# Optimization experiments

Hardware: AMD Instinct MI355X
Metric: run time of the kernel (lower is better)

The kernel has to match this reference:

```python
import jax, jax.numpy as jnp
import numpy as np
import itertools, math

MODES = 10
PHOTONS = 5
_IN_MODES_NP = np.arange(0, MODES, 2)  # input_state = [1,0,1,0,...]: photons in even modes
IN_MODES = jnp.asarray(_IN_MODES_NP)

# ---- Ryser's formula constants for 5x5 permanents (2^5 = 32 column subsets) ----
P = PHOTONS
_SUBS = np.array([[(s >> j) & 1 for j in range(P)] for s in range(1 << P)], dtype=np.float32)
_SIGNS = np.array([(-1.0) ** (P - bin(s).count('1')) for s in range(1 << P)], dtype=np.float32)
SUBS_C = jnp.asarray(_SUBS).astype(jnp.complex64)   # (32, P)
SIGNS = jnp.asarray(_SIGNS)                          # (32,)


def permanents(A):
    """Batched permanent via Ryser. A: (..., P, P) complex64 -> (...,) complex64."""
    # row sums over each column subset: (..., 32, P)
    rs = jnp.einsum('...rc,sc->...sr', A, SUBS_C)
    prods = jnp.prod(rs, axis=-1)            # (..., 32)
    return jnp.sum(prods * SIGNS, axis=-1)


def circuit_probs(theta, UL, UR, rows, norm):
    """Photonic circuit: U = UL @ diag(exp(i*theta)) @ UR, single photons in IN_MODES.
    theta: (N, m) real phases; rows: (K, P) output-row multisets; norm: 1/prod(occ!).
    Returns (N, K) Fock-state probabilities."""
    D = jnp.exp(1j * theta.astype(jnp.complex64))             # (N, m)
    U = jnp.einsum('ij,nj,jk->nik', UL, D, UR)                # (N, m, m)
    Ucols = U[:, :, IN_MODES]                                  # (N, m, P) input columns
    sub = Ucols[:, rows, :]                                    # (N, K, P, P)
    pm = permanents(sub)                                       # (N, K)
    return (pm.real ** 2 + pm.imag ** 2) * norm


def _cx(W):
    return (W[..., 0] + 1j * W[..., 1]).astype(jnp.complex64)


def setup_inputs() -> dict:
    key = jax.random.key(0)
    ks = jax.random.split(key, 8)
    N, input_dim, m, p = 256, 784, MODES, PHOTONS
    x = jax.random.normal(ks[0], (N, input_dim), jnp.float32)
    W_down = jax.random.normal(ks[1], (m, input_dim), jnp.float32) / np.sqrt(input_dim)
    b_down = jnp.zeros((m,), jnp.float32)

    def rand_unitary(k):
        a = jax.random.normal(k, (m, m, 2), jnp.float32)
        q, _ = jnp.linalg.qr((a[..., 0] + 1j * a[..., 1]).astype(jnp.complex64))
        return jnp.stack([q.real, q.imag], axis=-1).astype(jnp.float32)

    U1L, U1R, UfL, UfR = (rand_unitary(ks[i]) for i in range(2, 6))

    # circuit 1 keys: no_bunching -> C(10,5)=252 single-occupancy states
    keys1 = np.array(list(itertools.combinations(range(m), p)), dtype=np.int32)  # (252, 5)
    occ1 = np.zeros((len(keys1), m), dtype=np.float32)
    occ1[np.arange(len(keys1))[:, None], keys1] = 1.0   # occupancy mask (keys >= 1)
    # final circuit keys: bunching allowed -> C(14,5)=2002 multisets of modes
    rows2_np = np.array(list(itertools.combinations_with_replacement(range(m), p)), dtype=np.int32)
    norm2_np = np.array(
        [1.0 / np.prod([math.factorial(int(c)) for c in np.bincount(r, minlength=m)]) for r in rows2_np],
        dtype=np.float32)

    W_out = jax.random.normal(ks[6], (2, len(rows2_np)), jnp.float32) / np.sqrt(len(rows2_np))
    b_out = jnp.zeros((2,), jnp.float32)
    return {
        'x': x, 'W_down': W_down, 'b_down': b_down,
        'U1L': U1L, 'U1R': U1R, 'UfL': UfL, 'UfR': UfR,
        'W_out': W_out, 'b_out': b_out,
        'mask1': jnp.asarray(occ1), 'norm2': jnp.asarray(norm2_np),
        'rows1': jnp.asarray(keys1), 'rows2': jnp.asarray(rows2_np),
    }


def reference(x, W_down, b_down, U1L, U1R, UfL, UfR, W_out, b_out, mask1, norm2, rows1, rows2):
    h = x @ W_down.T + b_down            # downscaling_layer: (N, m)
    theta = h / jnp.pi                   # DivideByPi
    # quantum circuit 1 (no_bunching=True -> postselected/renormalized subspace)
    p1 = circuit_probs(theta, _cx(U1L), _cx(U1R), rows1, 1.0)       # (N, 252)
    p1 = p1 / jnp.sum(p1, axis=-1, keepdims=True)
    e1 = p1 @ mask1                       # marginalize_photon_presence: (N, m)
    # final quantum circuit (full Fock distribution, E=1)
    pf = circuit_probs(e1, _cx(UfL), _cx(UfR), rows2, norm2)        # (N, 2002)
    return pf @ W_out.T + b_out           # output_layer logits (N, 2)
```

## Files before the change

kernel.cpp:

```cpp
#include <hip/hip_runtime.h>
#include <hip/hip_bf16.h>


__device__ __forceinline__ float2 cxmul(float2 a, float2 b) {
    float2 r;
    r.x = fmaf(a.x, b.x, -(a.y * b.y));
    r.y = fmaf(a.x, b.y, a.y * b.x);
    return r;
}

__device__ __forceinline__ int Crt(int c, int k) {
    switch (k) {
        case 0:  return 1;
        case 1:  return c;
        case 2:  return (int)((unsigned)(c * (c - 1)) >> 1);
        case 3:  return (int)((unsigned)(c * (c - 1) * (c - 2)) / 6u);
        case 4:  return (int)((unsigned)(c * (c - 1) * (c - 2) * (c - 3)) / 24u);
        default: return (int)((unsigned)(c * (c - 1) * (c - 2) * (c - 3) * (c - 4)) / 120u);
    }
}

template<int D>
__device__ __forceinline__ void unrank_ms(int R, int (&m)[D]) {
#pragma unroll
    for (int i = D - 1; i >= 0; --i) {
        int c = i;
#pragma unroll
        for (int v = 1; v <= 9; ++v)
            c += (Crt(i + v, i + 1) <= R) ? 1 : 0;
        R -= Crt(c, i + 1);
        m[i] = c - i;
    }
}

template<int D>
__device__ __forceinline__ void build_edges(const int (&m)[D], unsigned (&e)[D]) {
    int c[D];
#pragma unroll
    for (int i = 0; i < D; ++i) c[i] = m[i] + i;
    int P[D];
    P[0] = 0;
#pragma unroll
    for (int j = 1; j < D; ++j) P[j] = P[j - 1] + Crt(c[j - 1], j);
    int S[D];
    S[D - 1] = 0;
#pragma unroll
    for (int j = D - 2; j >= 0; --j) S[j] = S[j + 1] + Crt(c[j + 1] - 1, j + 1);
#pragma unroll
    for (int j = 0; j < D; ++j) {
        bool valid = (j == 0) || (m[j] != m[j - 1]);
        unsigned edge = (((unsigned)(P[j] + S[j])) << 4) | (unsigned)m[j] | 0x80000000u;
        e[j] = valid ? edge : 0u;
    }
}

__device__ __forceinline__ float2 dp_acc(float2 acc, unsigned e, const float2* pbuf,
                                         const float2* B, int col) {
    if (e & 0x80000000u) {
        float2 p = pbuf[(e >> 4) & 0x3FFu];
        float2 b = B[(e & 15u) * 5 + col];
        acc.x = fmaf(b.x, p.x, acc.x);
        acc.x = fmaf(-b.y, p.y, acc.x);
        acc.y = fmaf(b.x, p.y, acc.y);
        acc.y = fmaf(b.y, p.x, acc.y);
    }
    return acc;
}

__global__ __launch_bounds__(1024) void k_fused(
    const float* __restrict__ x, const float* __restrict__ Wd, const float* __restrict__ bd,
    const float* __restrict__ U1L, const float* __restrict__ U1R,
    const float* __restrict__ UfL, const float* __restrict__ UfR,
    const float* __restrict__ Wout, const float* __restrict__ bout,
    const float* __restrict__ mask1, const float* __restrict__ norm2,
    const int* __restrict__ rows1, const int* __restrict__ rows2,
    float* __restrict__ out)
{
    const int n    = blockIdx.x;
    const int tid  = threadIdx.x;
    const int lane = tid & 63;
    const int wid  = tid >> 6;

    __shared__ float2 Bsh[50];
    __shared__ float2 buf1[220];
    __shared__ float2 buf2[715];
    __shared__ float  p1s[252];
    __shared__ float2 Dsh[10];
    __shared__ float  fred[16][2];

    int m5a[5];
#pragma unroll
    for (int j = 0; j < 5; ++j) m5a[j] = 0;
    if (tid < 252) {
#pragma unroll
        for (int j = 0; j < 5; ++j) m5a[j] = rows1[tid * 5 + j];
    }
    int m5b0[5];
#pragma unroll
    for (int j = 0; j < 5; ++j) m5b0[j] = rows2[tid * 5 + j];
    int m5b1[5];
#pragma unroll
    for (int j = 0; j < 5; ++j) m5b1[j] = 0;
    const bool has_p1 = (tid + 1024) < 2002;
    if (has_p1) {
#pragma unroll
        for (int j = 0; j < 5; ++j) m5b1[j] = rows2[(tid + 1024) * 5 + j];
    }

    if (wid < 10) {
        const float* xr = x + n * 784;
        const float* wr = Wd + wid * 784;
        float s = 0.f;
#pragma unroll
        for (int t = 0; t < 12; ++t) {
            const int k = lane + t * 64;
            s = fmaf(xr[k], wr[k], s);
        }
        if (lane < 16) {
            const int k = lane + 768;
            s = fmaf(xr[k], wr[k], s);
        }
#pragma unroll
        for (int off = 32; off > 0; off >>= 1) s += __shfl_xor(s, off, 64);
        if (lane == 0) {
            float h = s + bd[wid];
            float sn, cs;
            __sincosf(h * 0.31830988618379067154f, &sn, &cs);
            Dsh[wid] = make_float2(cs, sn);
        }
    }
    unsigned e2[2];
#pragma unroll
    for (int j = 0; j < 2; ++j) e2[j] = 0u;
    if (tid < 55)  { int m[2]; unrank_ms<2>(tid, m); build_edges<2>(m, e2); }
    __syncthreads();

    if (tid < 50) {
        const int i = tid / 5, cc = tid % 5, k = 2 * cc;
        float2 a = make_float2(0.f, 0.f);
#pragma unroll
        for (int j = 0; j < 10; ++j) {
            float2 ul = make_float2(U1L[(i * 10 + j) * 2], U1L[(i * 10 + j) * 2 + 1]);
            float2 ur = make_float2(U1R[(j * 10 + k) * 2], U1R[(j * 10 + k) * 2 + 1]);
            float2 t = cxmul(cxmul(ul, Dsh[j]), ur);
            a.x += t.x; a.y += t.y;
        }
        Bsh[tid] = a;
        if (cc == 0) buf1[i] = a;
    }
    __syncthreads();

    if (tid < 55) {
        float2 a = make_float2(0.f, 0.f);
#pragma unroll
        for (int j = 0; j < 2; ++j) a = dp_acc(a, e2[j], buf1, Bsh, 1);
        buf2[tid] = a;
    }
    unsigned e3[3];
#pragma unroll
    for (int j = 0; j < 3; ++j) e3[j] = 0u;
    if (tid < 220) { int m[3]; unrank_ms<3>(tid, m); build_edges<3>(m, e3); }
    __syncthreads();
    if (tid < 220) {
        float2 a = make_float2(0.f, 0.f);
#pragma unroll
        for (int j = 0; j < 3; ++j) a = dp_acc(a, e3[j], buf2, Bsh, 2);
        buf1[tid] = a;
    }
    unsigned e4[4];
#pragma unroll
    for (int j = 0; j < 4; ++j) e4[j] = 0u;
    if (tid < 715) { int m[4]; unrank_ms<4>(tid, m); build_edges<4>(m, e4); }
    __syncthreads();
    if (tid < 715) {
        float2 a = make_float2(0.f, 0.f);
#pragma unroll
        for (int j = 0; j < 4; ++j) a = dp_acc(a, e4[j], buf1, Bsh, 3);
        buf2[tid] = a;
    }
    unsigned e5a[5], e5b0[5], e5b1[5];
#pragma unroll
    for (int j = 0; j < 5; ++j) { e5a[j] = 0u; e5b1[j] = 0u; }
    if (tid < 252) { build_edges<5>(m5a, e5a); }
    build_edges<5>(m5b0, e5b0);
    if (has_p1) { build_edges<5>(m5b1, e5b1); }
    float fact0, fact1;
    {
        int f = 1, c = 1;
#pragma unroll
        for (int j = 1; j < 5; ++j) { c = (m5b0[j] == m5b0[j - 1]) ? c + 1 : 1; f *= c; }
        fact0 = (float)f;
        f = 1; c = 1;
#pragma unroll
        for (int j = 1; j < 5; ++j) { c = (m5b1[j] == m5b1[j - 1]) ? c + 1 : 1; f *= c; }
        fact1 = (float)f;
    }
    __syncthreads();
    if (tid < 252) {
        float2 a = make_float2(0.f, 0.f);
#pragma unroll
        for (int j = 0; j < 5; ++j) a = dp_acc(a, e5a[j], buf2, Bsh, 4);
        p1s[tid] = fmaf(a.x, a.x, a.y * a.y);
    }
    __syncthreads();

    if (wid < 10) {
        float sm = 0.f, st = 0.f;
        for (int p = lane; p < 252; p += 64) {
            const float pv = p1s[p];
            sm = fmaf(pv, mask1[p * 10 + wid], sm);
            st += pv;
        }
#pragma unroll
        for (int off = 32; off > 0; off >>= 1) {
            sm += __shfl_xor(sm, off, 64);
            st += __shfl_xor(st, off, 64);
        }
        if (lane == 0) {
            float e = sm / st;
            float sn, cs;
            __sincosf(e, &sn, &cs);
            Dsh[wid] = make_float2(cs, sn);
        }
    }
    __syncthreads();
    if (tid < 50) {
        const int i = tid / 5, cc = tid % 5, k = 2 * cc;
        float2 a = make_float2(0.f, 0.f);
#pragma unroll
        for (int j = 0; j < 10; ++j) {
            float2 ul = make_float2(UfL[(i * 10 + j) * 2], UfL[(i * 10 + j) * 2 + 1]);
            float2 ur = make_float2(UfR[(j * 10 + k) * 2], UfR[(j * 10 + k) * 2 + 1]);
            float2 t = cxmul(cxmul(ul, Dsh[j]), ur);
            a.x += t.x; a.y += t.y;
        }
        Bsh[tid] = a;
        if (cc == 0) buf1[i] = a;
    }
    __syncthreads();

    if (tid < 55) {
        float2 a = make_float2(0.f, 0.f);
#pragma unroll
        for (int j = 0; j < 2; ++j) a = dp_acc(a, e2[j], buf1, Bsh, 1);
        buf2[tid] = a;
    }
    __syncthreads();
    if (tid < 220) {
        float2 a = make_float2(0.f, 0.f);
#pragma unroll
        for (int j = 0; j < 3; ++j) a = dp_acc(a, e3[j], buf2, Bsh, 2);
        buf1[tid] = a;
    }
    __syncthreads();
    if (tid < 715) {
        float2 a = make_float2(0.f, 0.f);
#pragma unroll
        for (int j = 0; j < 4; ++j) a = dp_acc(a, e4[j], buf1, Bsh, 3);
        buf2[tid] = a;
    }
    __syncthreads();
    float f0 = 0.f, f1 = 0.f;
    {
        float2 a = make_float2(0.f, 0.f);
#pragma unroll
        for (int j = 0; j < 5; ++j) a = dp_acc(a, e5b0[j], buf2, Bsh, 4);
        const float pf = fmaf(a.x, a.x, a.y * a.y) * fact0;
        f0 = fmaf(pf, Wout[tid], f0);
        f1 = fmaf(pf, Wout[2002 + tid], f1);
    }
    if (has_p1) {
        float2 a = make_float2(0.f, 0.f);
#pragma unroll
        for (int j = 0; j < 5; ++j) a = dp_acc(a, e5b1[j], buf2, Bsh, 4);
        const float pf = fmaf(a.x, a.x, a.y * a.y) * fact1;
        f0 = fmaf(pf, Wout[tid + 1024], f0);
        f1 = fmaf(pf, Wout[2002 + tid + 1024], f1);
    }
#pragma unroll
    for (int off = 32; off > 0; off >>= 1) {
        f0 += __shfl_xor(f0, off, 64);
        f1 += __shfl_xor(f1, off, 64);
    }
    if (lane == 0) { fred[wid][0] = f0; fred[wid][1] = f1; }
    __syncthreads();
    if (tid < 2) {
        float a = bout[tid];
#pragma unroll
        for (int w = 0; w < 16; ++w) a += fred[w][tid];
        out[n * 2 + tid] = a;
    }
}

extern "C" void kernel_launch(void* const* d_in, const int* in_sizes, int n_in,
                              void* d_out, int out_size, void* d_ws, size_t ws_size,
                              hipStream_t stream) {
    const float* x     = (const float*)d_in[0];
    const float* Wd    = (const float*)d_in[1];
    const float* bd    = (const float*)d_in[2];
    const float* U1L   = (const float*)d_in[3];
    const float* U1R   = (const float*)d_in[4];
    const float* UfL   = (const float*)d_in[5];
    const float* UfR   = (const float*)d_in[6];
    const float* Wout  = (const float*)d_in[7];
    const float* bout  = (const float*)d_in[8];
    const float* mask1 = (const float*)d_in[9];
    const float* norm2 = (const float*)d_in[10];
    const int*   rows1 = (const int*)d_in[11];
    const int*   rows2 = (const int*)d_in[12];
    float* out = (float*)d_out;

    hipLaunchKernelGGL(k_fused, dim3(256), dim3(1024), 0, stream,
                       x, Wd, bd, U1L, U1R, UfL, UfR, Wout, bout,
                       mask1, norm2, rows1, rows2, out);
}
```

Baseline: 14.68 us.

## Collapse early permanent DP stages into one wavefront and prefetch weights

The first three DP stages (unitary column build, degree-2 and degree-3 partial permanents) now run inside wavefront 0 only, using wave barriers and LDS waitcnts instead of block-wide __syncthreads. This cuts several block barriers per circuit. W_out and mask1 values are preloaded into registers at kernel start so their global latency overlaps earlier work, and the downscale dot product uses four independent accumulators. The cost is serialized degree-3 work in one wave (4 iterations) plus more register pressure.

```diff
diff --git a/kernel.cpp b/kernel.cpp
--- a/kernel.cpp
+++ b/kernel.cpp
@@ -106,20 +106,34 @@
 #pragma unroll
         for (int j = 0; j < 5; ++j) m5b1[j] = rows2[(tid + 1024) * 5 + j];
     }
+    const float w0a = Wout[tid];
+    const float w1a = Wout[2002 + tid];
+    const float w0b = has_p1 ? Wout[tid + 1024] : 0.f;
+    const float w1b = has_p1 ? Wout[2002 + tid + 1024] : 0.f;
+    float mk[4];
+#pragma unroll
+    for (int t = 0; t < 4; ++t) mk[t] = 0.f;
+    if (wid < 10) {
+#pragma unroll
+        for (int t = 0; t < 4; ++t) {
+            const int p = lane + t * 64;
+            mk[t] = (p < 252) ? mask1[p * 10 + wid] : 0.f;
+        }
+    }
 
     if (wid < 10) {
         const float* xr = x + n * 784;
         const float* wr = Wd + wid * 784;
-        float s = 0.f;
-#pragma unroll
-        for (int t = 0; t < 12; ++t) {
-            const int k = lane + t * 64;
-            s = fmaf(xr[k], wr[k], s);
-        }
-        if (lane < 16) {
-            const int k = lane + 768;
-            s = fmaf(xr[k], wr[k], s);
-        }
+        float s0 = 0.f, s1 = 0.f, s2 = 0.f, s3 = 0.f;
+#pragma unroll
+        for (int t = 0; t < 12; t += 4) {
+            s0 = fmaf(xr[lane + t * 64],       wr[lane + t * 64],       s0);
+            s1 = fmaf(xr[lane + (t + 1) * 64], wr[lane + (t + 1) * 64], s1);
+            s2 = fmaf(xr[lane + (t + 2) * 64], wr[lane + (t + 2) * 64], s2);
+            s3 = fmaf(xr[lane + (t + 3) * 64], wr[lane + (t + 3) * 64], s3);
+        }
+        if (lane < 16) s0 = fmaf(xr[lane + 768], wr[lane + 768], s0);
+        float s = (s0 + s1) + (s2 + s3);
 #pragma unroll
         for (int off = 32; off > 0; off >>= 1) s += __shfl_xor(s, off, 64);
         if (lane == 0) {
@@ -135,49 +149,47 @@
     if (tid < 55)  { int m[2]; unrank_ms<2>(tid, m); build_edges<2>(m, e2); }
     __syncthreads();
 
-    if (tid < 50) {
-        const int i = tid / 5, cc = tid % 5, k = 2 * cc;
-        float2 a = make_float2(0.f, 0.f);
-#pragma unroll
-        for (int j = 0; j < 10; ++j) {
-            float2 ul = make_float2(U1L[(i * 10 + j) * 2], U1L[(i * 10 + j) * 2 + 1]);
-            float2 ur = make_float2(U1R[(j * 10 + k) * 2], U1R[(j * 10 + k) * 2 + 1]);
-            float2 t = cxmul(cxmul(ul, Dsh[j]), ur);
-            a.x += t.x; a.y += t.y;
-        }
-        Bsh[tid] = a;
-        if (cc == 0) buf1[i] = a;
-    }
-    __syncthreads();
-
-    if (tid < 55) {
-        float2 a = make_float2(0.f, 0.f);
-#pragma unroll
-        for (int j = 0; j < 2; ++j) a = dp_acc(a, e2[j], buf1, Bsh, 1);
-        buf2[tid] = a;
-    }
-    unsigned e3[3];
-#pragma unroll
-    for (int j = 0; j < 3; ++j) e3[j] = 0u;
-    if (tid < 220) { int m[3]; unrank_ms<3>(tid, m); build_edges<3>(m, e3); }
-    __syncthreads();
-    if (tid < 220) {
-        float2 a = make_float2(0.f, 0.f);
-#pragma unroll
-        for (int j = 0; j < 3; ++j) a = dp_acc(a, e3[j], buf2, Bsh, 2);
-        buf1[tid] = a;
+    if (wid == 0) {
+        if (lane < 50) {
+            const int i = lane / 5, cc = lane % 5, k = 2 * cc;
+            float2 a = make_float2(0.f, 0.f);
+#pragma unroll
+            for (int j = 0; j < 10; ++j) {
+                float2 ul = make_float2(U1L[(i * 10 + j) * 2], U1L[(i * 10 + j) * 2 + 1]);
+                float2 ur = make_float2(U1R[(j * 10 + k) * 2], U1R[(j * 10 + k) * 2 + 1]);
+                float2 t = cxmul(cxmul(ul, Dsh[j]), ur);
+                a.x += t.x; a.y += t.y;
+            }
+            Bsh[lane] = a;
+            if (cc == 0) buf1[i] = a;
+        }
+        asm volatile("s_waitcnt lgkmcnt(0)" ::: "memory");
+        __builtin_amdgcn_wave_barrier();
+        if (lane < 55) {
+            float2 a = make_float2(0.f, 0.f);
+#pragma unroll
+            for (int j = 0; j < 2; ++j) a = dp_acc(a, e2[j], buf1, Bsh, 1);
+            buf2[lane] = a;
+        }
+        asm volatile("s_waitcnt lgkmcnt(0)" ::: "memory");
+        __builtin_amdgcn_wave_barrier();
+#pragma unroll
+        for (int kk = 0; kk < 4; ++kk) {
+            const int o = lane + kk * 64;
+            if (o < 220) {
+                int m[3]; unrank_ms<3>(o, m);
+                unsigned e3t[3]; build_edges<3>(m, e3t);
+                float2 a = make_float2(0.f, 0.f);
+#pragma unroll
+                for (int j = 0; j < 3; ++j) a = dp_acc(a, e3t[j], buf2, Bsh, 2);
+                buf1[o] = a;
+            }
+        }
     }
     unsigned e4[4];
 #pragma unroll
     for (int j = 0; j < 4; ++j) e4[j] = 0u;
     if (tid < 715) { int m[4]; unrank_ms<4>(tid, m); build_edges<4>(m, e4); }
-    __syncthreads();
-    if (tid < 715) {
-        float2 a = make_float2(0.f, 0.f);
-#pragma unroll
-        for (int j = 0; j < 4; ++j) a = dp_acc(a, e4[j], buf1, Bsh, 3);
-        buf2[tid] = a;
-    }
     unsigned e5a[5], e5b0[5], e5b1[5];
 #pragma unroll
     for (int j = 0; j < 5; ++j) { e5a[j] = 0u; e5b1[j] = 0u; }
@@ -196,6 +208,14 @@
         fact1 = (float)f;
     }
     __syncthreads();
+
+    if (tid < 715) {
+        float2 a = make_float2(0.f, 0.f);
+#pragma unroll
+        for (int j = 0; j < 4; ++j) a = dp_acc(a, e4[j], buf1, Bsh, 3);
+        buf2[tid] = a;
+    }
+    __syncthreads();
     if (tid < 252) {
         float2 a = make_float2(0.f, 0.f);
 #pragma unroll
@@ -206,10 +226,14 @@
 
     if (wid < 10) {
         float sm = 0.f, st = 0.f;
-        for (int p = lane; p < 252; p += 64) {
-            const float pv = p1s[p];
-            sm = fmaf(pv, mask1[p * 10 + wid], sm);
-            st += pv;
+#pragma unroll
+        for (int t = 0; t < 4; ++t) {
+            const int p = lane + t * 64;
+            if (p < 252) {
+                const float pv = p1s[p];
+                sm = fmaf(pv, mk[t], sm);
+                st += pv;
+            }
         }
 #pragma unroll
         for (int off = 32; off > 0; off >>= 1) {
@@ -224,35 +248,46 @@
         }
     }
     __syncthreads();
-    if (tid < 50) {
-        const int i = tid / 5, cc = tid % 5, k = 2 * cc;
-        float2 a = make_float2(0.f, 0.f);
-#pragma unroll
-        for (int j = 0; j < 10; ++j) {
-            float2 ul = make_float2(UfL[(i * 10 + j) * 2], UfL[(i * 10 + j) * 2 + 1]);
-            float2 ur = make_float2(UfR[(j * 10 + k) * 2], UfR[(j * 10 + k) * 2 + 1]);
-            float2 t = cxmul(cxmul(ul, Dsh[j]), ur);
-            a.x += t.x; a.y += t.y;
-        }
-        Bsh[tid] = a;
-        if (cc == 0) buf1[i] = a;
-    }
-    __syncthreads();
-
-    if (tid < 55) {
-        float2 a = make_float2(0.f, 0.f);
-#pragma unroll
-        for (int j = 0; j < 2; ++j) a = dp_acc(a, e2[j], buf1, Bsh, 1);
-        buf2[tid] = a;
-    }
-    __syncthreads();
-    if (tid < 220) {
-        float2 a = make_float2(0.f, 0.f);
-#pragma unroll
-        for (int j = 0; j < 3; ++j) a = dp_acc(a, e3[j], buf2, Bsh, 2);
-        buf1[tid] = a;
-    }
-    __syncthreads();
+
+    if (wid == 0) {
+        if (lane < 50) {
+            const int i = lane / 5, cc = lane % 5, k = 2 * cc;
+            float2 a = make_float2(0.f, 0.f);
+#pragma unroll
+            for (int j = 0; j < 10; ++j) {
+                float2 ul = make_float2(UfL[(i * 10 + j) * 2], UfL[(i * 10 + j) * 2 + 1]);
+                float2 ur = make_float2(UfR[(j * 10 + k) * 2], UfR[(j * 10 + k) * 2 + 1]);
+                float2 t = cxmul(cxmul(ul, Dsh[j]), ur);
+                a.x += t.x; a.y += t.y;
+            }
+            Bsh[lane] = a;
+            if (cc == 0) buf1[i] = a;
+        }
+        asm volatile("s_waitcnt lgkmcnt(0)" ::: "memory");
+        __builtin_amdgcn_wave_barrier();
+        if (lane < 55) {
+            float2 a = make_float2(0.f, 0.f);
+#pragma unroll
+            for (int j = 0; j < 2; ++j) a = dp_acc(a, e2[j], buf1, Bsh, 1);
+            buf2[lane] = a;
+        }
+        asm volatile("s_waitcnt lgkmcnt(0)" ::: "memory");
+        __builtin_amdgcn_wave_barrier();
+#pragma unroll
+        for (int kk = 0; kk < 4; ++kk) {
+            const int o = lane + kk * 64;
+            if (o < 220) {
+                int m[3]; unrank_ms<3>(o, m);
+                unsigned e3t[3]; build_edges<3>(m, e3t);
+                float2 a = make_float2(0.f, 0.f);
+#pragma unroll
+                for (int j = 0; j < 3; ++j) a = dp_acc(a, e3t[j], buf2, Bsh, 2);
+                buf1[o] = a;
+            }
+        }
+    }
+    __syncthreads();
+
     if (tid < 715) {
         float2 a = make_float2(0.f, 0.f);
 #pragma unroll
@@ -266,16 +301,16 @@
 #pragma unroll
         for (int j = 0; j < 5; ++j) a = dp_acc(a, e5b0[j], buf2, Bsh, 4);
         const float pf = fmaf(a.x, a.x, a.y * a.y) * fact0;
-        f0 = fmaf(pf, Wout[tid], f0);
-        f1 = fmaf(pf, Wout[2002 + tid], f1);
+        f0 = fmaf(pf, w0a, f0);
+        f1 = fmaf(pf, w1a, f1);
     }
     if (has_p1) {
         float2 a = make_float2(0.f, 0.f);
 #pragma unroll
         for (int j = 0; j < 5; ++j) a = dp_acc(a, e5b1[j], buf2, Bsh, 4);
         const float pf = fmaf(a.x, a.x, a.y * a.y) * fact1;
-        f0 = fmaf(pf, Wout[tid + 1024], f0);
-        f1 = fmaf(pf, Wout[2002 + tid + 1024], f1);
+        f0 = fmaf(pf, w0b, f0);
+        f1 = fmaf(pf, w1b, f1);
     }
 #pragma unroll
     for (int off = 32; off > 0; off >>= 1) {
```

New measurement: 16.32 us. +11.2%, slower.
